# Optimization experiments

Hardware: AMD Instinct MI355X
Metric: run time of the kernel (lower is better)

Reference implementation:

```python
import jax, jax.numpy as jnp
import numpy as np

NUM_GROUPS = 32
EPS = 1e-5


def group_norm(x, scale, bias):
    # x: [b, c, h, w]
    b, c, h, w = x.shape
    xg = x.reshape(b, NUM_GROUPS, c // NUM_GROUPS, h, w)
    mean = jnp.mean(xg, axis=(2, 3, 4), keepdims=True)
    var = jnp.var(xg, axis=(2, 3, 4), keepdims=True)
    xg = (xg - mean) * jax.lax.rsqrt(var + EPS)
    xn = xg.reshape(b, c, h, w)
    return xn * scale[None, :, None, None] + bias[None, :, None, None]


def conv1x1(x, w, b):
    # x: [b, c_in, h, w], w: [c_out, c_in], b: [c_out]
    return jnp.einsum('bchw,dc->bdhw', x, w) + b[None, :, None, None]


def setup_inputs() -> dict:
    key = jax.random.key(0)
    ks = jax.random.split(key, 11)
    B, C, H, W = 16, 512, 32, 32
    s = 1.0 / np.sqrt(C)
    inp = {
        'x': jax.random.normal(ks[0], (B, C, H, W), jnp.float32),
        'gn_scale': jnp.ones((C,), jnp.float32),
        'gn_bias': jnp.zeros((C,), jnp.float32),
        'wq': jax.random.normal(ks[1], (C, C), jnp.float32) * s,
        'bq': jnp.zeros((C,), jnp.float32),
        'wk': jax.random.normal(ks[2], (C, C), jnp.float32) * s,
        'bk': jnp.zeros((C,), jnp.float32),
        'wv': jax.random.normal(ks[3], (C, C), jnp.float32) * s,
        'bv': jnp.zeros((C,), jnp.float32),
        'wp': jax.random.normal(ks[4], (C, C), jnp.float32) * s,
        'bp': jnp.zeros((C,), jnp.float32),
    }
    return inp


def reference(x, gn_scale, gn_bias, wq, bq, wk, bk, wv, bv, wp, bp):
    b, c, h, w = x.shape
    xn = group_norm(x, gn_scale, gn_bias)
    q = conv1x1(xn, wq, bq).reshape(b, c, h * w)  # [b, c, n]
    k = conv1x1(xn, wk, bk).reshape(b, c, h * w)
    v = conv1x1(xn, wv, bv).reshape(b, c, h * w)
    # attn[b, i, j] = sum_c q[b, c, i] * k[b, c, j]
    attn = jnp.einsum('bci,bcj->bij', q, k) * (c ** -0.5)
    A = jax.nn.softmax(attn, axis=-1)
    # out[b, c, i] = sum_j A[b, i, j] * v[b, c, j]
    out = jnp.einsum('bij,bcj->bci', A, v).reshape(b, c, h, w)
    scores = conv1x1(out, wp, bp)
    return x + scores
```

## Files before the change

### kernel.cpp

```cpp
#include <hip/hip_runtime.h>

typedef __bf16 bf16x8 __attribute__((ext_vector_type(8)));
typedef float  f32x4  __attribute__((ext_vector_type(4)));

__device__ __forceinline__ unsigned short f2bf(float f) {
    union { float f; unsigned int u; } x; x.f = f;
    unsigned int r = (x.u + 0x7FFFu + ((x.u >> 16) & 1u)) >> 16;
    return (unsigned short)r;
}

typedef const __attribute__((address_space(1))) unsigned short gu16;
typedef __attribute__((address_space(3)))       unsigned short lu16;
__device__ __forceinline__ void gl_lds16(const unsigned short* g, unsigned short* l) {
    __builtin_amdgcn_global_load_lds((gu16*)g, (lu16*)l, 16, 0, 0);
}

template<int NT, int BMH>
__device__ __forceinline__ void stage8g(
    const unsigned short* __restrict__ Ab, int lda,
    const unsigned short* __restrict__ Bb, int ldb,
    unsigned short* LB, int s, int wave, int lane)
{
    if (s >= 4 * NT) return;
    const int tau  = s >> 2;
    const int pi   = s & 3;
    const int half = pi & 1;
    const int kc   = tau * 64 + (((lane & 7) ^ ((lane >> 5) << 1)) << 3);
    if (pi >= 2) {
        unsigned short* dst = LB + (tau & 1) * (BMH * 8192) + half * (BMH * 4096) + wave * 512;
        const int R = half * (BMH * 64) + wave * 8 + (lane >> 3);
        gl_lds16(Ab + (long)R * lda + kc, dst);
        if constexpr (BMH == 2) gl_lds16(Ab + (long)(R + 64) * lda + kc, dst + 4096);
    } else {
        unsigned short* dst = LB + (BMH * 16384) + (tau & 1) * 16384 + half * 8192 + wave * 512;
        const int R = half * 128 + wave * 8 + (lane >> 3);
        gl_lds16(Bb + (long)R * ldb + kc, dst);
        gl_lds16(Bb + (long)(R + 64) * ldb + kc, dst + 4096);
    }
}

template<int NT, int BMH>
__device__ __forceinline__ void gemm8_core(
    const unsigned short* __restrict__ Ab, int lda,
    const unsigned short* __restrict__ Bb, int ldb,
    f32x4 (&acc)[4 * BMH][4], unsigned short* LB)
{
    const int tid  = threadIdx.x;
    const int lane = tid & 63;
    const int wave = tid >> 6;
    const int wM   = wave >> 2;
    const int wN   = wave & 3;
    const int l16  = lane & 15;
    const int quad = lane >> 4;
    const int ckx  = quad ^ (((l16 >> 2) & 1) << 1);
    const int aoff = wM * (BMH * 4096) + l16 * 64 + ckx * 8;
    const int boff = BMH * 16384 + (wN >> 1) * 8192 + ((wN & 1) * 64 + l16) * 64 + ckx * 8;

#define VMW do { if constexpr (BMH == 2) asm volatile("s_waitcnt vmcnt(6)" ::: "memory"); \
                 else                    asm volatile("s_waitcnt vmcnt(5)" ::: "memory"); } while (0)

    #pragma unroll
    for (int s = 0; s < 7; ++s)
        stage8g<NT, BMH>(Ab, lda, Bb, ldb, LB, s, wave, lane);
    VMW;
    __builtin_amdgcn_s_barrier();
    __builtin_amdgcn_sched_barrier(0);

    bf16x8 af[2 * BMH][2], bf[4][2];

#define RD_A(buf, mh)                                                         \
    _Pragma("unroll")                                                         \
    for (int m = 0; m < 2 * BMH; ++m)                                         \
        _Pragma("unroll")                                                     \
        for (int kk = 0; kk < 2; ++kk)                                        \
            af[m][kk] = *(const bf16x8*)&LB[(buf) * (BMH * 8192) + aoff + ((mh) * 2 * BMH + m) * 1024 + kk * 32];
#define RD_B(buf)                                                             \
    _Pragma("unroll")                                                         \
    for (int n = 0; n < 4; ++n)                                               \
        _Pragma("unroll")                                                     \
        for (int kk = 0; kk < 2; ++kk)                                        \
            bf[n][kk] = *(const bf16x8*)&LB[(buf) * 16384 + boff + n * 1024 + kk * 32];
#define MF(mh, nh)                                                            \
    __builtin_amdgcn_s_setprio(1);                                            \
    _Pragma("unroll")                                                         \
    for (int m = 0; m < 2 * BMH; ++m)                                         \
        _Pragma("unroll")                                                     \
        for (int n = 0; n < 2; ++n)                                           \
            _Pragma("unroll")                                                 \
            for (int kk = 0; kk < 2; ++kk)                                    \
                acc[(mh) * 2 * BMH + m][(nh) * 2 + n] = __builtin_amdgcn_mfma_f32_16x16x32_bf16( \
                    af[m][kk], bf[(nh) * 2 + n][kk], acc[(mh) * 2 * BMH + m][(nh) * 2 + n], 0, 0, 0); \
    __builtin_amdgcn_s_setprio(0);
#define BARS do { __builtin_amdgcn_s_barrier(); __builtin_amdgcn_sched_barrier(0); } while (0)
#define LGW  do { asm volatile("s_waitcnt lgkmcnt(0)" ::: "memory"); __builtin_amdgcn_sched_barrier(0); } while (0)

    const int NITER = NT / 2;
    for (int i = 0; i < NITER; ++i) {
        const int s0 = 6 + 8 * i;
        RD_B(0) RD_A(0, 0)
        stage8g<NT, BMH>(Ab, lda, Bb, ldb, LB, s0 + 1, wave, lane);
        BARS; LGW;
        MF(0, 0)
        BARS;
        stage8g<NT, BMH>(Ab, lda, Bb, ldb, LB, s0 + 2, wave, lane);
        BARS;
        MF(0, 1)
        BARS;
        RD_A(0, 1)
        stage8g<NT, BMH>(Ab, lda, Bb, ldb, LB, s0 + 3, wave, lane);
        BARS; LGW;
        MF(1, 0)
        BARS;
        stage8g<NT, BMH>(Ab, lda, Bb, ldb, LB, s0 + 4, wave, lane);
        BARS;
        MF(1, 1)
        if (i == NITER - 1) { asm volatile("s_waitcnt vmcnt(0)" ::: "memory"); }
        else                { VMW; }
        BARS;
        RD_B(1) RD_A(1, 0)
        stage8g<NT, BMH>(Ab, lda, Bb, ldb, LB, s0 + 5, wave, lane);
        BARS; LGW;
        MF(0, 0)
        BARS;
        stage8g<NT, BMH>(Ab, lda, Bb, ldb, LB, s0 + 6, wave, lane);
        BARS;
        MF(0, 1)
        BARS;
        RD_A(1, 1)
        stage8g<NT, BMH>(Ab, lda, Bb, ldb, LB, s0 + 7, wave, lane);
        BARS; LGW;
        MF(1, 0)
        BARS;
        stage8g<NT, BMH>(Ab, lda, Bb, ldb, LB, s0 + 8, wave, lane);
        BARS;
        MF(1, 1)
        if (i < NITER - 1) { VMW; }
        BARS;
    }
#undef RD_A
#undef RD_B
#undef MF
#undef BARS
#undef LGW
#undef VMW
}

__global__ __launch_bounds__(512, 2) void p8_k(
    const unsigned short* __restrict__ qT,
    const unsigned short* __restrict__ kT,
    unsigned short* __restrict__ Sb,
    float* __restrict__ lsum,
    float alpha)
{
    __shared__ __align__(16) unsigned short LB[65536];
    const int z = blockIdx.z;
    const unsigned short* Ab = qT + (long)z * 524288 + (long)(blockIdx.y * 256) * 512;
    const unsigned short* Bb = kT + (long)z * 524288 + (long)(blockIdx.x * 256) * 512;
    f32x4 acc[8][4] = {};
    gemm8_core<8, 2>(Ab, 512, Bb, 512, acc, LB);

    const int lane = threadIdx.x & 63, wave = threadIdx.x >> 6;
    const int wM = wave >> 2, wN = wave & 3;
    const int l16 = lane & 15, quad = lane >> 4;
    const int gm0 = blockIdx.y * 256 + wM * 128;
    const int gn0 = blockIdx.x * 256 + wN * 64;
    unsigned short* scr = LB + wave * 8192;

    float rs[8][4];
    #pragma unroll
    for (int mi = 0; mi < 8; ++mi) { rs[mi][0] = rs[mi][1] = rs[mi][2] = rs[mi][3] = 0.f; }
    #pragma unroll
    for (int mi = 0; mi < 8; ++mi)
        #pragma unroll
        for (int ni = 0; ni < 4; ++ni) {
            f32x4 v = acc[mi][ni];
            #pragma unroll
            for (int r = 0; r < 4; ++r) {
                float e = __expf(v[r] * alpha);
                rs[mi][r] += e;
                const int row = mi * 16 + quad * 4 + r;
                const int col = ni * 16 + l16;
                scr[row * 64 + (((col >> 3) ^ (row & 7)) << 3) + (col & 7)] = f2bf(e);
            }
        }
    #pragma unroll
    for (int mi = 0; mi < 8; ++mi)
        #pragma unroll
        for (int r = 0; r < 4; ++r) {
            float s = rs[mi][r];
            s += __shfl_xor(s, 1); s += __shfl_xor(s, 2);
            s += __shfl_xor(s, 4); s += __shfl_xor(s, 8);
            if (l16 == 0)
                atomicAdd(&lsum[(long)z * 1024 + gm0 + mi * 16 + quad * 4 + r], s);
        }
    unsigned short* dst = Sb + (long)z * 1048576;
    #pragma unroll
    for (int it = 0; it < 16; ++it) {
        const int row = it * 8 + (lane >> 3);
        const int ck  = lane & 7;
        uint4 vv = *(uint4*)&scr[row * 64 + ((ck ^ (row & 7)) << 3)];
        *(uint4*)&dst[(long)(gm0 + row) * 1024 + gn0 + ck * 8] = vv;
    }
}

__global__ __launch_bounds__(512, 2) void qkv8_k(
    const unsigned short* __restrict__ Wqkv,
    const unsigned short* __restrict__ xnT,
    unsigned short* __restrict__ qT,
    unsigned short* __restrict__ kT,
    unsigned short* __restrict__ vB,
    const float* __restrict__ bqkv)
{
    __shared__ __align__(16) unsigned short LB[49152];
    const int z = blockIdx.z;
    const unsigned short* Ab = Wqkv + (long)(blockIdx.y * 128) * 512;
    const unsigned short* Bb = xnT + (long)z * 524288 + (long)(blockIdx.x * 256) * 512;
    f32x4 acc[4][4] = {};
    gemm8_core<8, 1>(Ab, 512, Bb, 512, acc, LB);

    const int lane = threadIdx.x & 63, wave = threadIdx.x >> 6;
    const int wM = wave >> 2, wN = wave & 3;
    const int l16 = lane & 15, quad = lane >> 4;
    const int gm0 = blockIdx.y * 128 + wM * 64;
    const int gn0 = blockIdx.x * 256 + wN * 64;
    const int mat = blockIdx.y >> 2;
    const int ml0 = gm0 & 511;
    const long zb = (long)z * 524288;
    unsigned short* scr = LB + wave * 4096;

    if (mat == 2) {
        #pragma unroll
        for (int mi = 0; mi < 4; ++mi)
            #pragma unroll
            for (int ni = 0; ni < 4; ++ni) {
                f32x4 v = acc[mi][ni];
                #pragma unroll
                for (int r = 0; r < 4; ++r) {
                    const int ml = mi * 16 + quad * 4 + r;
                    const int nc = ni * 2 + (l16 >> 3);
                    scr[ml * 64 + ((nc ^ (ml & 7)) * 8) + (l16 & 7)] = f2bf(v[r] + bqkv[gm0 + ml]);
                }
            }
        const int ch2 = lane & 7, rr = lane >> 3;
        unsigned short* dst = vB + zb + gn0 + ch2 * 8;
        #pragma unroll
        for (int it = 0; it < 8; ++it) {
            const int ml = rr + it * 8;
            uint4 vv = *(uint4*)&scr[ml * 64 + ((ch2 ^ (ml & 7)) * 8)];
            *(uint4*)(dst + (long)(ml0 + ml) * 1024) = vv;
        }
    } else {
        unsigned short* dstm = (mat == 0) ? qT : kT;
        #pragma unroll
        for (int mi = 0; mi < 4; ++mi)
            #pragma unroll
            for (int ni = 0; ni < 4; ++ni) {
                f32x4 v = acc[mi][ni];
                const int nl = ni * 16 + l16;
                const int ch = mi * 2 + (quad >> 1);
                const int m4 = gm0 + mi * 16 + quad * 4;
                ushort4 p;
                p.x = f2bf(v[0] + bqkv[m4 + 0]);
                p.y = f2bf(v[1] + bqkv[m4 + 1]);
                p.z = f2bf(v[2] + bqkv[m4 + 2]);
                p.w = f2bf(v[3] + bqkv[m4 + 3]);
                *(ushort4*)&scr[nl * 64 + ((ch ^ (nl & 7)) * 8) + (quad & 1) * 4] = p;
            }
        const int ch2 = lane & 7, rr = lane >> 3;
        unsigned short* dst = dstm + zb + ml0 + ch2 * 8;
        #pragma unroll
        for (int it = 0; it < 8; ++it) {
            const int nl = rr + it * 8;
            uint4 vv = *(uint4*)&scr[nl * 64 + ((ch2 ^ (nl & 7)) * 8)];
            *(uint4*)(dst + (long)(gn0 + nl) * 512) = vv;
        }
    }
}

__global__ __launch_bounds__(512, 2) void av8_k(
    const unsigned short* __restrict__ vB,
    const unsigned short* __restrict__ Sb,
    unsigned short* __restrict__ OT,
    const float* __restrict__ Lb)
{
    __shared__ __align__(16) unsigned short LB[49152];
    const int z = blockIdx.z;
    const unsigned short* Ab = vB + (long)z * 524288 + (long)(blockIdx.y * 128) * 1024;
    const unsigned short* Bb = Sb + (long)z * 1048576 + (long)(blockIdx.x * 256) * 1024;
    f32x4 acc[4][4] = {};
    gemm8_core<16, 1>(Ab, 1024, Bb, 1024, acc, LB);

    const int lane = threadIdx.x & 63, wave = threadIdx.x >> 6;
    const int wM = wave >> 2, wN = wave & 3;
    const int l16 = lane & 15, quad = lane >> 4;
    const int gm0 = blockIdx.y * 128 + wM * 64;
    const int gn0 = blockIdx.x * 256 + wN * 64;
    unsigned short* scr = LB + wave * 4096;

    #pragma unroll
    for (int mi = 0; mi < 4; ++mi)
        #pragma unroll
        for (int ni = 0; ni < 4; ++ni) {
            f32x4 v = acc[mi][ni];
            const float invl = 1.f / Lb[(long)z * 1024 + gn0 + ni * 16 + l16];
            const int nl = ni * 16 + l16;
            const int ch = mi * 2 + (quad >> 1);
            ushort4 p;
            p.x = f2bf(v[0] * invl); p.y = f2bf(v[1] * invl);
            p.z = f2bf(v[2] * invl); p.w = f2bf(v[3] * invl);
            *(ushort4*)&scr[nl * 64 + ((ch ^ (nl & 7)) * 8) + (quad & 1) * 4] = p;
        }
    const int ch2 = lane & 7, rr = lane >> 3;
    unsigned short* dst = OT + (long)z * 524288 + gm0 + ch2 * 8;
    #pragma unroll
    for (int it = 0; it < 8; ++it) {
        const int nl = rr + it * 8;
        uint4 vv = *(uint4*)&scr[nl * 64 + ((ch2 ^ (nl & 7)) * 8)];
        *(uint4*)(dst + (long)(gn0 + nl) * 512) = vv;
    }
}

__device__ __forceinline__ void stage_tiles(
    const unsigned short* __restrict__ Ab, int lda,
    const unsigned short* __restrict__ Bb, int ldb,
    int k0, unsigned short* Ad, unsigned short* Bd,
    int wave, int r0, int c0)
{
    gl_lds16(Ab + (long)r0 * lda + c0 + k0,        Ad + wave * 512);
    gl_lds16(Ab + (long)(r0 + 64) * lda + c0 + k0, Ad + 2048 + wave * 512);
    gl_lds16(Bb + (long)r0 * ldb + c0 + k0,        Bd + wave * 512);
    gl_lds16(Bb + (long)(r0 + 64) * ldb + c0 + k0, Bd + 2048 + wave * 512);
}

__device__ __forceinline__ void gemm_core_db(
    const unsigned short* __restrict__ Ab, int lda,
    const unsigned short* __restrict__ Bb, int ldb,
    int K, f32x4 (&acc)[4][4],
    unsigned short* As, unsigned short* Bs)
{
    const int tid  = threadIdx.x;
    const int lane = tid & 63;
    const int wave = tid >> 6;
    const int wm   = (wave >> 1) * 64;
    const int wn   = (wave & 1) * 64;
    const int l16  = lane & 15;
    const int quad = lane >> 4;

    const int r0 = wave * 16 + (lane >> 2);
    const int c0 = ((lane & 3) ^ ((lane >> 3) & 3)) * 8;

    stage_tiles(Ab, lda, Bb, ldb, 0, As, Bs, wave, r0, c0);

    const int sw8 = ((l16 >> 1) & 3) * 8;

    int sel = 0;
    for (int k0 = 0; k0 < K; k0 += 32) {
        __syncthreads();
        if (k0 + 32 < K)
            stage_tiles(Ab, lda, Bb, ldb, k0 + 32,
                        As + (sel ^ 1) * 4096, Bs + (sel ^ 1) * 4096, wave, r0, c0);

        const unsigned short* Ap = As + sel * 4096;
        const unsigned short* Bp = Bs + sel * 4096;
        bf16x8 af[4], bfr[4];
        #pragma unroll
        for (int mi = 0; mi < 4; mi++)
            af[mi] = *(const bf16x8*)&Ap[(wm + mi * 16 + l16) * 32 + ((quad * 8) ^ sw8)];
        #pragma unroll
        for (int ni = 0; ni < 4; ni++)
            bfr[ni] = *(const bf16x8*)&Bp[(wn + ni * 16 + l16) * 32 + ((quad * 8) ^ sw8)];
        #pragma unroll
        for (int mi = 0; mi < 4; mi++)
            #pragma unroll
            for (int ni = 0; ni < 4; ni++)
                acc[mi][ni] = __builtin_amdgcn_mfma_f32_16x16x32_bf16(af[mi], bfr[ni], acc[mi][ni], 0, 0, 0);
        sel ^= 1;
    }
}

__global__ __launch_bounds__(256) void fin_k(
    const unsigned short* __restrict__ Wp,
    const unsigned short* __restrict__ OTb,
    float* __restrict__ out,
    const float* __restrict__ bias,
    const float* __restrict__ resid)
{
    __shared__ __align__(16) unsigned short LB[16384];
    unsigned short* As = LB;
    unsigned short* Bs = LB + 8192;

    const unsigned short* Ab = Wp + (long)(blockIdx.y * 128) * 512;
    const unsigned short* Bb = OTb + (long)blockIdx.z * 524288 + (long)(blockIdx.x * 128) * 512;

    f32x4 acc[4][4] = {};
    gemm_core_db(Ab, 512, Bb, 512, 512, acc, As, Bs);

    const int lane = threadIdx.x & 63;
    const int wave = threadIdx.x >> 6;
    const int l16  = lane & 15;
    const int quad = lane >> 4;
    const int mb = blockIdx.y * 128 + (wave >> 1) * 64;
    const int nb = blockIdx.x * 128 + (wave & 1) * 64;

    #pragma unroll
    for (int mi = 0; mi < 4; mi++) {
        #pragma unroll
        for (int ni = 0; ni < 4; ni++) {
            f32x4 v = acc[mi][ni];
            const int m0 = mb + mi * 16 + quad * 4;
            const int n  = nb + ni * 16 + l16;
            const long base = (long)blockIdx.z * 524288;
            #pragma unroll
            for (int r = 0; r < 4; r++) {
                float val = v[r] + bias[m0 + r] + resid[base + (long)(m0 + r) * 1024 + n];
                out[base + (long)(m0 + r) * 1024 + n] = val;
            }
        }
    }
}

__global__ __launch_bounds__(256) void gnw_k(
    const float* __restrict__ x, const float* __restrict__ gsc,
    const float* __restrict__ gbi, unsigned short* __restrict__ xnT,
    const float* __restrict__ w0, const float* __restrict__ w1,
    const float* __restrict__ w2, const float* __restrict__ w3,
    const float* __restrict__ b0, const float* __restrict__ b1,
    const float* __restrict__ b2,
    unsigned short* __restrict__ wout, float* __restrict__ bqkv,
    float* __restrict__ lsum)
{
    __shared__ __align__(16) unsigned short ln[16 * 1024];
    __shared__ float red[8];
    const int bid = blockIdx.x;
    const int tid = threadIdx.x;

    if (bid >= 512) {
        const int j = bid - 512;
        const int m = j >> 8;
        const int i = (j & 255) * 256 + tid;
        if (m == 4) {
            if (i < 384) {
                const int which = i >> 7, off = i & 127;
                const float* src = (which == 0) ? b0 : (which == 1) ? b1 : b2;
                ((float4*)bqkv)[i] = ((const float4*)src)[off];
            }
            if (i < 16384) lsum[i] = 0.f;
            return;
        }
        const float* src = (m == 0) ? w0 : (m == 1) ? w1 : (m == 2) ? w2 : w3;
        float4 v = ((const float4*)src)[i];
        ushort4 o; o.x = f2bf(v.x); o.y = f2bf(v.y); o.z = f2bf(v.z); o.w = f2bf(v.w);
        ((ushort4*)(wout + (long)m * 262144))[i] = o;
        return;
    }

    const int b = bid >> 5, g = bid & 31;
    const int lane = tid & 63, wv = tid >> 6;

    const float4* x4 = (const float4*)(x + ((long)b * 512 + g * 16) * 1024);
    float4 vals[16];
    float s = 0.f, ss = 0.f;
    #pragma unroll
    for (int i = 0; i < 16; i++) {
        float4 v = x4[tid + i * 256];
        vals[i] = v;
        s  += v.x + v.y + v.z + v.w;
        ss += v.x * v.x + v.y * v.y + v.z * v.z + v.w * v.w;
    }
    for (int o = 32; o; o >>= 1) { s += __shfl_down(s, o); ss += __shfl_down(ss, o); }
    if (lane == 0) { red[wv * 2] = s; red[wv * 2 + 1] = ss; }
    __syncthreads();
    const float S  = red[0] + red[2] + red[4] + red[6];
    const float SS = red[1] + red[3] + red[5] + red[7];
    const float mean = S * (1.f / 16384.f);
    const float var  = SS * (1.f / 16384.f) - mean * mean;
    const float inv  = rsqrtf(var + 1e-5f);

    #pragma unroll
    for (int i = 0; i < 16; i++) {
        const int idx = tid + i * 256;
        const int c   = idx >> 8;
        const float sc = gsc[g * 16 + c] * inv;
        const float bi = gbi[g * 16 + c] - mean * sc;
        float4 v = vals[i];
        ushort4 p;
        p.x = f2bf(v.x * sc + bi); p.y = f2bf(v.y * sc + bi);
        p.z = f2bf(v.z * sc + bi); p.w = f2bf(v.w * sc + bi);
        ((ushort4*)ln)[idx] = p;
    }
    __syncthreads();

    unsigned short* op = xnT + (long)b * 1024 * 512 + g * 16;
    for (int rep = 0; rep < 4; rep++) {
        const int n = rep * 256 + tid;
        union { unsigned short u[16]; uint4 v[2]; } t;
        #pragma unroll
        for (int c = 0; c < 16; c++) t.u[c] = ln[c * 1024 + n];
        *(uint4*)&op[(long)n * 512]     = t.v[0];
        *(uint4*)&op[(long)n * 512 + 8] = t.v[1];
    }
}

extern "C" void kernel_launch(void* const* d_in, const int* in_sizes, int n_in,
                              void* d_out, int out_size, void* d_ws, size_t ws_size,
                              hipStream_t stream)
{
    const float* x   = (const float*)d_in[0];
    const float* gsc = (const float*)d_in[1];
    const float* gbi = (const float*)d_in[2];
    const float* wq  = (const float*)d_in[3];
    const float* bq  = (const float*)d_in[4];
    const float* wk  = (const float*)d_in[5];
    const float* bk  = (const float*)d_in[6];
    const float* wv  = (const float*)d_in[7];
    const float* bv  = (const float*)d_in[8];
    const float* wp  = (const float*)d_in[9];
    const float* bp  = (const float*)d_in[10];
    float* out = (float*)d_out;

    char* ws = (char*)d_ws;
    unsigned short* xnT = (unsigned short*)(ws);
    unsigned short* qT  = (unsigned short*)(ws + 16777216);
    unsigned short* kT  = (unsigned short*)(ws + 33554432);
    unsigned short* vB  = (unsigned short*)(ws + 50331648);
    unsigned short* Sb  = (unsigned short*)(ws + 67108864);
    unsigned short* Wb  = (unsigned short*)(ws + 100663296);
    float*          bqkv= (float*)        (ws + 102760448);
    float*          Lb  = (float*)        (ws + 102768640);
    unsigned short* OT  = xnT;

    gnw_k<<<1792, 256, 0, stream>>>(x, gsc, gbi, xnT,
                                    wq, wk, wv, wp, bq, bk, bv, Wb, bqkv, Lb);

    qkv8_k<<<dim3(4, 12, 16), 512, 0, stream>>>(Wb, xnT, qT, kT, vB, bqkv);

    p8_k<<<dim3(4, 4, 16), 512, 0, stream>>>(qT, kT, Sb, Lb, 0.044194173824159216f);

    av8_k<<<dim3(4, 4, 16), 512, 0, stream>>>(vB, Sb, OT, Lb);

    fin_k<<<dim3(8, 4, 16), 256, 0, stream>>>(Wb + 786432, OT, out, bp, x);
}
```

Baseline: 219.4 us.

## Use triple-buffered LDS GEMM core for QKV and AV kernels

Replaces the double-buffered 8-phase GEMM core in the QKV projection and attention-times-V kernels with a new three-stage LDS ring that prefetches tiles two K-steps ahead. Each step splits the MFMA work into two halves, issuing B and A loads for step t+2 between them. The aim is to hide more global-load latency behind the matrix math. It grows shared memory from 96KB to 144KB per block, which may cut the two-blocks-per-CU occupancy the launch bounds request, and adds barriers before the epilogue scratch reuse.

After: 221.9 us. Within noise of the previous version (+1.1%).

```diff
diff --git a/kernel.cpp b/kernel.cpp
--- a/kernel.cpp
+++ b/kernel.cpp
@@ -13,6 +13,106 @@
 typedef __attribute__((address_space(3)))       unsigned short lu16;
 __device__ __forceinline__ void gl_lds16(const unsigned short* g, unsigned short* l) {
     __builtin_amdgcn_global_load_lds((gu16*)g, (lu16*)l, 16, 0, 0);
+}
+
+__device__ __forceinline__ void stageB23(
+    const unsigned short* __restrict__ Bb, int ldb,
+    unsigned short* LB, int t, int buf, int wave, int lane)
+{
+    const int kc = t * 64 + (((lane & 7) ^ ((lane >> 5) << 1)) << 3);
+    unsigned short* dst = LB + buf * 24576 + 8192 + wave * 512;
+    const int R = wave * 8 + (lane >> 3);
+    gl_lds16(Bb + (long)R * ldb + kc,         dst);
+    gl_lds16(Bb + (long)(R + 64) * ldb + kc,  dst + 4096);
+    gl_lds16(Bb + (long)(R + 128) * ldb + kc, dst + 8192);
+    gl_lds16(Bb + (long)(R + 192) * ldb + kc, dst + 12288);
+}
+__device__ __forceinline__ void stageA23(
+    const unsigned short* __restrict__ Ab, int lda,
+    unsigned short* LB, int t, int buf, int wave, int lane)
+{
+    const int kc = t * 64 + (((lane & 7) ^ ((lane >> 5) << 1)) << 3);
+    unsigned short* dst = LB + buf * 24576 + wave * 512;
+    const int R = wave * 8 + (lane >> 3);
+    gl_lds16(Ab + (long)R * lda + kc,        dst);
+    gl_lds16(Ab + (long)(R + 64) * lda + kc, dst + 4096);
+}
+
+template<int NT>
+__device__ __forceinline__ void gemm23_core(
+    const unsigned short* __restrict__ Ab, int lda,
+    const unsigned short* __restrict__ Bb, int ldb,
+    f32x4 (&acc)[4][4], unsigned short* LB)
+{
+    const int tid  = threadIdx.x;
+    const int lane = tid & 63;
+    const int wave = tid >> 6;
+    const int wM   = wave >> 2;
+    const int wN   = wave & 3;
+    const int l16  = lane & 15;
+    const int quad = lane >> 4;
+    const int ckx  = quad ^ (((l16 >> 2) & 1) << 1);
+    const int aoff = (wM * 64 + l16) * 64 + ckx * 8;
+    const int boff = 8192 + (wN * 64 + l16) * 64 + ckx * 8;
+
+    stageB23(Bb, ldb, LB, 0, 0, wave, lane);
+    stageA23(Ab, lda, LB, 0, 0, wave, lane);
+    stageB23(Bb, ldb, LB, 1, 1, wave, lane);
+    stageA23(Ab, lda, LB, 1, 1, wave, lane);
+    asm volatile("s_waitcnt vmcnt(6)" ::: "memory");
+    __builtin_amdgcn_s_barrier();
+    __builtin_amdgcn_sched_barrier(0);
+
+    bf16x8 af[2][2], bf[4][2];
+
+#define RD_A23(buf, mh)                                                       \
+    _Pragma("unroll")                                                         \
+    for (int m = 0; m < 2; ++m)                                               \
+        _Pragma("unroll")                                                     \
+        for (int kk = 0; kk < 2; ++kk)                                        \
+            af[m][kk] = *(const bf16x8*)&LB[(buf) * 24576 + aoff + ((mh) * 2 + m) * 1024 + kk * 32];
+#define RD_B23(buf)                                                           \
+    _Pragma("unroll")                                                         \
+    for (int n = 0; n < 4; ++n)                                               \
+        _Pragma("unroll")                                                     \
+        for (int kk = 0; kk < 2; ++kk)                                        \
+            bf[n][kk] = *(const bf16x8*)&LB[(buf) * 24576 + boff + n * 1024 + kk * 32];
+#define MF23(mh)                                                              \
+    __builtin_amdgcn_s_setprio(1);                                            \
+    _Pragma("unroll")                                                         \
+    for (int m = 0; m < 2; ++m)                                               \
+        _Pragma("unroll")                                                     \
+        for (int n = 0; n < 4; ++n)                                           \
+            _Pragma("unroll")                                                 \
+            for (int kk = 0; kk < 2; ++kk)                                    \
+                acc[(mh) * 2 + m][n] = __builtin_amdgcn_mfma_f32_16x16x32_bf16( \
+                    af[m][kk], bf[n][kk], acc[(mh) * 2 + m][n], 0, 0, 0);     \
+    __builtin_amdgcn_s_setprio(0);
+#define BARS23 do { __builtin_amdgcn_s_barrier(); __builtin_amdgcn_sched_barrier(0); } while (0)
+#define LGW23  do { asm volatile("s_waitcnt lgkmcnt(0)" ::: "memory"); __builtin_amdgcn_sched_barrier(0); } while (0)
+
+    int b = 0, b2 = 2;
+    for (int t = 0; t < NT; ++t) {
+        RD_B23(b) RD_A23(b, 0)
+        if (t + 2 < NT) stageB23(Bb, ldb, LB, t + 2, b2, wave, lane);
+        BARS23; LGW23;
+        MF23(0)
+        BARS23;
+        RD_A23(b, 1)
+        if (t + 2 < NT) stageA23(Ab, lda, LB, t + 2, b2, wave, lane);
+        BARS23; LGW23;
+        MF23(1)
+        if (t + 2 < NT) { asm volatile("s_waitcnt vmcnt(6)" ::: "memory"); }
+        else            { asm volatile("s_waitcnt vmcnt(0)" ::: "memory"); }
+        BARS23;
+        b  = (b == 2)  ? 0 : b + 1;
+        b2 = (b2 == 2) ? 0 : b2 + 1;
+    }
+#undef RD_A23
+#undef RD_B23
+#undef MF23
+#undef BARS23
+#undef LGW23
 }
 
 template<int NT, int BMH>
@@ -211,12 +311,12 @@
     unsigned short* __restrict__ vB,
     const float* __restrict__ bqkv)
 {
-    __shared__ __align__(16) unsigned short LB[49152];
+    __shared__ __align__(16) unsigned short LB[73728];
     const int z = blockIdx.z;
     const unsigned short* Ab = Wqkv + (long)(blockIdx.y * 128) * 512;
     const unsigned short* Bb = xnT + (long)z * 524288 + (long)(blockIdx.x * 256) * 512;
     f32x4 acc[4][4] = {};
-    gemm8_core<8, 1>(Ab, 512, Bb, 512, acc, LB);
+    gemm23_core<8>(Ab, 512, Bb, 512, acc, LB);
 
     const int lane = threadIdx.x & 63, wave = threadIdx.x >> 6;
     const int wM = wave >> 2, wN = wave & 3;
@@ -241,6 +341,7 @@
                     scr[ml * 64 + ((nc ^ (ml & 7)) * 8) + (l16 & 7)] = f2bf(v[r] + bqkv[gm0 + ml]);
                 }
             }
+        __builtin_amdgcn_s_barrier();
         const int ch2 = lane & 7, rr = lane >> 3;
         unsigned short* dst = vB + zb + gn0 + ch2 * 8;
         #pragma unroll
@@ -266,6 +367,7 @@
                 p.w = f2bf(v[3] + bqkv[m4 + 3]);
                 *(ushort4*)&scr[nl * 64 + ((ch ^ (nl & 7)) * 8) + (quad & 1) * 4] = p;
             }
+        __builtin_amdgcn_s_barrier();
         const int ch2 = lane & 7, rr = lane >> 3;
         unsigned short* dst = dstm + zb + ml0 + ch2 * 8;
         #pragma unroll
@@ -283,12 +385,12 @@
     unsigned short* __restrict__ OT,
     const float* __restrict__ Lb)
 {
-    __shared__ __align__(16) unsigned short LB[49152];
+    __shared__ __align__(16) unsigned short LB[73728];
     const int z = blockIdx.z;
     const unsigned short* Ab = vB + (long)z * 524288 + (long)(blockIdx.y * 128) * 1024;
     const unsigned short* Bb = Sb + (long)z * 1048576 + (long)(blockIdx.x * 256) * 1024;
     f32x4 acc[4][4] = {};
-    gemm8_core<16, 1>(Ab, 1024, Bb, 1024, acc, LB);
+    gemm23_core<16>(Ab, 1024, Bb, 1024, acc, LB);
 
     const int lane = threadIdx.x & 63, wave = threadIdx.x >> 6;
     const int wM = wave >> 2, wN = wave & 3;
@@ -310,6 +412,7 @@
             p.z = f2bf(v[2] * invl); p.w = f2bf(v[3] * invl);
             *(ushort4*)&scr[nl * 64 + ((ch ^ (nl & 7)) * 8) + (quad & 1) * 4] = p;
         }
+    __builtin_amdgcn_s_barrier();
     const int ch2 = lane & 7, rr = lane >> 3;
     unsigned short* dst = OT + (long)z * 524288 + gm0 + ch2 * 8;
     #pragma unroll
```
